# Kernel tuning notes

Measured on AMD Instinct MI355X. Metric: run time of the kernel, lower is better.

Reference implementation:

```python
import jax, jax.numpy as jnp
import numpy as np


def setup_inputs() -> dict:
    key = jax.random.key(0)
    ks = jax.random.split(key, 8)
    B, IN, P, D1, D2, C = 1024, 4096, 512, 8, 16, 4
    H1, H2 = D1 * P, D2 * P
    H3 = H2 // 4
    return {
        "data_omics": jax.random.normal(ks[0], (B, IN), jnp.float32),
        "comp": jax.random.randint(ks[1], (IN, P), 0, 2, jnp.int32),
        "fc1_w": jax.random.normal(ks[2], (IN, H1), jnp.float32) * (2.0 / (IN + H1)) ** 0.5,
        "fc1_b": jax.random.uniform(ks[3], (H1,), jnp.float32),
        "fc2_w": jax.random.normal(ks[4], (H1, H2), jnp.float32) * (2.0 / (H1 + H2)) ** 0.5,
        "fc2_b": jax.random.uniform(ks[5], (H2,), jnp.float32),
        "w3": jax.random.normal(ks[6], (H2, H3), jnp.float32) * (2.0 / (H2 + H3)) ** 0.5,
        "b3": jnp.zeros((H3,), jnp.float32),
        "w4": jax.random.normal(ks[7], (H3, C), jnp.float32) * (2.0 / (H3 + C)) ** 0.5,
        "b4": jnp.zeros((C,), jnp.float32),
    }


def reference(data_omics, comp, fc1_w, fc1_b, fc2_w, fc2_b, w3, b3, w4, b4):
    P = comp.shape[1]
    D1 = fc1_w.shape[1] // P          # dim_per_path_1
    D2 = fc2_w.shape[1] // P          # dim_per_path_2
    # mask_1: [input_dim, D1*P] gene->pathway membership, repeated per hidden unit
    mask_1 = jnp.repeat(comp.astype(fc1_w.dtype), D1, axis=1)
    # mask_2: block-diagonal [D1*P, D2*P] with D1xD2 blocks of ones
    mask_2 = jnp.kron(jnp.eye(P, dtype=fc2_w.dtype), jnp.ones((D1, D2), fc2_w.dtype))
    out = jnp.matmul(data_omics, fc1_w * mask_1) + fc1_b      # [B, D1*P]
    out = jnp.matmul(out, fc2_w * mask_2) + fc2_b             # [B, D2*P]
    h = jax.nn.relu(jnp.matmul(out, w3) + b3)                 # dropout is eval no-op
    logits = jnp.matmul(h, w4) + b4                           # [B, num_classes]
    return logits
```

## Files before the change

kernel.cpp:

```cpp
#include <hip/hip_runtime.h>
#include <hip/hip_bf16.h>
#include <cstdint>
#include <cstddef>

typedef __bf16 bf16_t;
typedef __bf16 bf16x8 __attribute__((ext_vector_type(8)));
typedef float f32x4 __attribute__((ext_vector_type(4)));

#define AS1(p) ((const __attribute__((address_space(1))) void*)(p))
#define AS3(p) ((__attribute__((address_space(3))) void*)(p))

struct bf16x4_s { bf16_t x, y, z, w; };

__global__ __launch_bounds__(256) void k_transpose(const float* __restrict__ W,
                                                   const int* __restrict__ comp,
                                                   bf16_t* __restrict__ Bt,
                                                   int K, int N, int Pc) {
  __shared__ float tile[64][65];
  const int k0 = blockIdx.x * 64;
  const int n0 = blockIdx.y * 64;
  const int t = threadIdx.x;
  const int c = t & 63;
  const int r0 = t >> 6;
#pragma unroll
  for (int i = 0; i < 16; ++i) {
    int r = r0 + i * 4;
    float v = W[(size_t)(k0 + r) * N + n0 + c];
    v *= (float)comp[(size_t)(k0 + r) * Pc + ((n0 + c) >> 3)];
    tile[r][c] = v;
  }
  __syncthreads();
#pragma unroll
  for (int i = 0; i < 16; ++i) {
    int r = r0 + i * 4;
    Bt[(size_t)(n0 + r) * K + k0 + c] = (bf16_t)tile[c][r];
  }
}

__global__ __launch_bounds__(256) void k_w23(const float* __restrict__ fc2w,
                                             const float* __restrict__ w3,
                                             const float* __restrict__ b2,
                                             bf16_t* __restrict__ W23t,
                                             float* __restrict__ b23) {
  __shared__ float w3s[128][65];
  const int n0 = blockIdx.x * 64;
  const int pb = blockIdx.y * 8;
  const int tid = threadIdx.x;
  const int c = tid & 63, q = tid >> 6;
#pragma unroll
  for (int i = 0; i < 32; ++i) {
    int rr = i * 4 + q;
    w3s[rr][c] = w3[(size_t)(pb * 16 + rr) * 2048 + n0 + c];
  }
  __syncthreads();
  const int pp = c >> 3;
  const int k1 = pb * 8 + c;
  const int p = pb + pp;
  float f2[16];
  const float4* frp = (const float4*)(fc2w + (size_t)k1 * 8192 + (size_t)p * 16);
#pragma unroll
  for (int t4 = 0; t4 < 4; ++t4) {
    float4 v = frp[t4];
    f2[t4 * 4 + 0] = v.x; f2[t4 * 4 + 1] = v.y; f2[t4 * 4 + 2] = v.z; f2[t4 * 4 + 3] = v.w;
  }
#pragma unroll
  for (int i = 0; i < 16; ++i) {
    int nn = i * 4 + q;
    float s = 0.f;
#pragma unroll
    for (int d2 = 0; d2 < 16; ++d2) {
      int d2r = (d2 + 2 * pp) & 15;
      s += f2[d2r] * w3s[pp * 16 + d2r][nn];
    }
    W23t[(size_t)(n0 + nn) * 4096 + k1] = (bf16_t)s;
  }
  float bp = 0.f;
  for (int rr = q * 32; rr < q * 32 + 32; ++rr)
    bp += b2[pb * 16 + rr] * w3s[rr][c];
  atomicAdd(&b23[n0 + c], bp);
}

template<int MI, int NI, bool AF32>
__global__ __launch_bounds__(256, 2) void k_gemm_sk(const void* __restrict__ Av,
                                                    const bf16_t* __restrict__ Bt,
                                                    float* __restrict__ P,
                                                    int M, int N, int K, int ksub) {
  constexpr int BM = MI * 32;
  constexpr int BN = NI * 32;
  constexpr int BK = 32;
  __shared__ bf16_t As[BM][BK];
  __shared__ bf16_t Bs[BN][BK];
  const int tid = threadIdx.x;
  const int wave = tid >> 6;
  const int lane = tid & 63;
  const int m0 = blockIdx.y * BM;
  const int n0 = blockIdx.x * BN;
  const int kbase = blockIdx.z * ksub;
  const int wm = (wave >> 1) * (MI * 16);
  const int wn = (wave & 1) * (NI * 16);
  const int lrow = lane >> 2;
  const int lk = (lane & 3) * 8;
  const int fr = lane & 15;
  const int fkb = (lane >> 4) * 8;

  f32x4 acc[MI][NI] = {};
  const int nkt = ksub / BK;
  for (int kt = 0; kt < nkt; ++kt) {
    const int k0 = kbase + kt * BK;
    if constexpr (AF32) {
      const float* Af = (const float*)Av;
      for (int i = wave; i < BM / 16; i += 4) {
        const float* g = Af + (size_t)(m0 + i * 16 + lrow) * K + k0 + lk;
        float4 a0 = *(const float4*)g;
        float4 a1 = *(const float4*)(g + 4);
        bf16x8 v;
        v[0] = (bf16_t)a0.x; v[1] = (bf16_t)a0.y; v[2] = (bf16_t)a0.z; v[3] = (bf16_t)a0.w;
        v[4] = (bf16_t)a1.x; v[5] = (bf16_t)a1.y; v[6] = (bf16_t)a1.z; v[7] = (bf16_t)a1.w;
        *reinterpret_cast<bf16x8*>(&As[i * 16 + lrow][lk]) = v;
      }
    } else {
      const bf16_t* Ab = (const bf16_t*)Av;
      for (int i = wave; i < BM / 16; i += 4) {
        const bf16_t* g = Ab + (size_t)(m0 + i * 16 + lrow) * K + k0 + lk;
        __builtin_amdgcn_global_load_lds(AS1(g), AS3(&As[i * 16][0]), 16, 0, 0);
      }
    }
    for (int i = wave; i < BN / 16; i += 4) {
      const bf16_t* g = Bt + (size_t)(n0 + i * 16 + lrow) * K + k0 + lk;
      __builtin_amdgcn_global_load_lds(AS1(g), AS3(&Bs[i * 16][0]), 16, 0, 0);
    }
    __syncthreads();

    bf16x8 af[MI], bfr[NI];
#pragma unroll
    for (int mi = 0; mi < MI; ++mi)
      af[mi] = *reinterpret_cast<const bf16x8*>(&As[wm + mi * 16 + fr][fkb]);
#pragma unroll
    for (int ni = 0; ni < NI; ++ni)
      bfr[ni] = *reinterpret_cast<const bf16x8*>(&Bs[wn + ni * 16 + fr][fkb]);
#pragma unroll
    for (int mi = 0; mi < MI; ++mi)
#pragma unroll
      for (int ni = 0; ni < NI; ++ni)
        acc[mi][ni] = __builtin_amdgcn_mfma_f32_16x16x32_bf16(af[mi], bfr[ni], acc[mi][ni], 0, 0, 0);
    __syncthreads();
  }

  float* Po = P + (size_t)blockIdx.z * ((size_t)M * N);
  const int fq = lane >> 4;
#pragma unroll
  for (int mi = 0; mi < MI; ++mi)
#pragma unroll
    for (int ni = 0; ni < NI; ++ni) {
      const int col = n0 + wn + ni * 16 + fr;
#pragma unroll
      for (int j = 0; j < 4; ++j) {
        const int row = m0 + wm + mi * 16 + fq * 4 + j;
        Po[(size_t)row * N + col] = acc[mi][ni][j];
      }
    }
}

template<int S, bool RELU, bool B2>
__global__ __launch_bounds__(256) void k_reduce(const float* __restrict__ P, size_t sz,
                                                const float* __restrict__ bias1,
                                                const float* __restrict__ bias2,
                                                bf16_t* __restrict__ out, int N) {
  const size_t i = (size_t)blockIdx.x * 256 + threadIdx.x;
  const size_t off = i * 4;
  float4 a = *(const float4*)(P + off);
#pragma unroll
  for (int s = 1; s < S; ++s) {
    float4 t = *(const float4*)(P + (size_t)s * sz + off);
    a.x += t.x; a.y += t.y; a.z += t.z; a.w += t.w;
  }
  const int col = (int)(off & (size_t)(N - 1));
  const float4 b1 = *(const float4*)(bias1 + col);
  a.x += b1.x; a.y += b1.y; a.z += b1.z; a.w += b1.w;
  if (B2) {
    const float4 b2v = *(const float4*)(bias2 + col);
    a.x += b2v.x; a.y += b2v.y; a.z += b2v.z; a.w += b2v.w;
  }
  if (RELU) {
    a.x = fmaxf(a.x, 0.f); a.y = fmaxf(a.y, 0.f);
    a.z = fmaxf(a.z, 0.f); a.w = fmaxf(a.w, 0.f);
  }
  bf16x4_s o{(bf16_t)a.x, (bf16_t)a.y, (bf16_t)a.z, (bf16_t)a.w};
  reinterpret_cast<bf16x4_s*>(out)[i] = o;
}

__global__ __launch_bounds__(256) void k_head(const bf16_t* __restrict__ h,
                                              const float* __restrict__ W4,
                                              const float* __restrict__ b4,
                                              float* __restrict__ out) {
  const int b = blockIdx.x;
  const int n = threadIdx.x >> 6;
  const int lane = threadIdx.x & 63;
  float s = 0.f;
  for (int k = lane; k < 2048; k += 64)
    s += (float)h[(size_t)b * 2048 + k] * W4[k * 4 + n];
#pragma unroll
  for (int off = 32; off; off >>= 1) s += __shfl_down(s, off);
  if (lane == 0) out[b * 4 + n] = s + b4[n];
}

extern "C" void kernel_launch(void* const* d_in, const int* in_sizes, int n_in,
                              void* d_out, int out_size, void* d_ws, size_t ws_size,
                              hipStream_t stream) {
  const float* data  = (const float*)d_in[0];
  const int*   comp  = (const int*)d_in[1];
  const float* fc1_w = (const float*)d_in[2];
  const float* fc1_b = (const float*)d_in[3];
  const float* fc2_w = (const float*)d_in[4];
  const float* fc2_b = (const float*)d_in[5];
  const float* w3    = (const float*)d_in[6];
  const float* b3    = (const float*)d_in[7];
  const float* w4    = (const float*)d_in[8];
  const float* b4    = (const float*)d_in[9];
  float* logits = (float*)d_out;

  char* ws = (char*)d_ws;
  bf16_t* Bt1  = (bf16_t*)(ws);
  bf16_t* out1 = (bf16_t*)(ws);
  bf16_t* W23t = (bf16_t*)(ws + 8388608);
  float*  b23  = (float*)(ws + 25165824);
  bf16_t* hbuf = (bf16_t*)(ws + 25174016);
  float*  P    = (float*)(ws + 33554432);

  k_transpose<<<dim3(64, 64), 256, 0, stream>>>(fc1_w, comp, Bt1, 4096, 4096, 512);
  k_gemm_sk<4, 4, true><<<dim3(32, 8, 2), 256, 0, stream>>>(data, Bt1, P, 1024, 4096, 4096, 2048);
  k_reduce<2, false, false><<<4096, 256, 0, stream>>>(P, (size_t)1024 * 4096, fc1_b, nullptr, out1, 4096);
  hipMemsetAsync(b23, 0, 8192, stream);
  k_w23<<<dim3(32, 64), 256, 0, stream>>>(fc2_w, w3, fc2_b, W23t, b23);
  k_gemm_sk<4, 4, false><<<dim3(16, 8, 4), 256, 0, stream>>>(out1, W23t, P, 1024, 2048, 4096, 1024);
  k_reduce<4, true, true><<<2048, 256, 0, stream>>>(P, (size_t)1024 * 2048, b23, b3, hbuf, 2048);
  k_head<<<1024, 256, 0, stream>>>(hbuf, w4, b4, logits);
}
```

Before: 458.5 us.

## Double-buffer GEMM LDS tiles, pre-cast input to bf16, deepen split-K

The split-K GEMM now double-buffers its A and B tiles in LDS, issuing the next tile's global loads before the MFMA work on the current tile. This drops one barrier per k-step and raises MFMA priority with s_setprio. When the workspace is large enough, the fp32 input is first cast to bf16 in a separate kernel so both GEMMs use the direct global-to-LDS load path. Split-K depth doubles in both GEMMs for more parallelism, at the cost of more partial-sum traffic in the reduce kernels and twice the LDS per block.

```diff
diff --git a/kernel.cpp b/kernel.cpp
--- a/kernel.cpp
+++ b/kernel.cpp
@@ -11,6 +11,16 @@
 #define AS3(p) ((__attribute__((address_space(3))) void*)(p))
 
 struct bf16x4_s { bf16_t x, y, z, w; };
+
+__global__ __launch_bounds__(256) void k_cast_bf16(const float4* __restrict__ in,
+                                                   bf16x4_s* __restrict__ out, int n4) {
+  int i = blockIdx.x * 256 + threadIdx.x;
+  if (i < n4) {
+    float4 v = in[i];
+    bf16x4_s o{(bf16_t)v.x, (bf16_t)v.y, (bf16_t)v.z, (bf16_t)v.w};
+    out[i] = o;
+  }
+}
 
 __global__ __launch_bounds__(256) void k_transpose(const float* __restrict__ W,
                                                    const int* __restrict__ comp,
@@ -81,69 +91,114 @@
 }
 
 template<int MI, int NI, bool AF32>
-__global__ __launch_bounds__(256, 2) void k_gemm_sk(const void* __restrict__ Av,
-                                                    const bf16_t* __restrict__ Bt,
-                                                    float* __restrict__ P,
-                                                    int M, int N, int K, int ksub) {
-  constexpr int BM = MI * 32;
-  constexpr int BN = NI * 32;
-  constexpr int BK = 32;
-  __shared__ bf16_t As[BM][BK];
-  __shared__ bf16_t Bs[BN][BK];
-  const int tid = threadIdx.x;
-  const int wave = tid >> 6;
-  const int lane = tid & 63;
-  const int m0 = blockIdx.y * BM;
-  const int n0 = blockIdx.x * BN;
+__global__ __launch_bounds__(256, AF32 ? 2 : 4)
+void k_gemm_sk(const void* __restrict__ Av,
+               const bf16_t* __restrict__ Bt,
+               float* __restrict__ P,
+               int M, int N, int K, int ksub) {
+  constexpr int BM = MI * 32, BN = NI * 32, BK = 32;
+  constexpr int AIT = BM / 64;
+  constexpr int BIT = BN / 64;
+  __shared__ bf16_t As[2][BM][BK];
+  __shared__ bf16_t Bs[2][BN][BK];
+  const int tid = threadIdx.x, wave = tid >> 6, lane = tid & 63;
+  const int m0 = blockIdx.y * BM, n0 = blockIdx.x * BN;
   const int kbase = blockIdx.z * ksub;
-  const int wm = (wave >> 1) * (MI * 16);
-  const int wn = (wave & 1) * (NI * 16);
-  const int lrow = lane >> 2;
-  const int lk = (lane & 3) * 8;
-  const int fr = lane & 15;
-  const int fkb = (lane >> 4) * 8;
+  const int wm = (wave >> 1) * (MI * 16), wn = (wave & 1) * (NI * 16);
+  const int lrow = lane >> 2, lk = (lane & 3) * 8;
+  const int fr = lane & 15, fkb = (lane >> 4) * 8;
+  const float* Af = (const float*)Av;
+  const bf16_t* Ab = (const bf16_t*)Av;
 
   f32x4 acc[MI][NI] = {};
   const int nkt = ksub / BK;
+
+  if constexpr (AF32) {
+#pragma unroll
+    for (int ii = 0; ii < AIT; ++ii) {
+      const int i = wave + ii * 4;
+      const float* g = Af + (size_t)(m0 + i * 16 + lrow) * K + kbase + lk;
+      float4 x = *(const float4*)g, y = *(const float4*)(g + 4);
+      bf16x8 v;
+      v[0] = (bf16_t)x.x; v[1] = (bf16_t)x.y; v[2] = (bf16_t)x.z; v[3] = (bf16_t)x.w;
+      v[4] = (bf16_t)y.x; v[5] = (bf16_t)y.y; v[6] = (bf16_t)y.z; v[7] = (bf16_t)y.w;
+      *reinterpret_cast<bf16x8*>(&As[0][i * 16 + lrow][lk]) = v;
+    }
+  } else {
+#pragma unroll
+    for (int ii = 0; ii < AIT; ++ii) {
+      const int i = wave + ii * 4;
+      const bf16_t* g = Ab + (size_t)(m0 + i * 16 + lrow) * K + kbase + lk;
+      __builtin_amdgcn_global_load_lds(AS1(g), AS3(&As[0][i * 16][0]), 16, 0, 0);
+    }
+  }
+#pragma unroll
+  for (int ii = 0; ii < BIT; ++ii) {
+    const int i = wave + ii * 4;
+    const bf16_t* g = Bt + (size_t)(n0 + i * 16 + lrow) * K + kbase + lk;
+    __builtin_amdgcn_global_load_lds(AS1(g), AS3(&Bs[0][i * 16][0]), 16, 0, 0);
+  }
+  __syncthreads();
+
+  int cur = 0;
   for (int kt = 0; kt < nkt; ++kt) {
-    const int k0 = kbase + kt * BK;
-    if constexpr (AF32) {
-      const float* Af = (const float*)Av;
-      for (int i = wave; i < BM / 16; i += 4) {
-        const float* g = Af + (size_t)(m0 + i * 16 + lrow) * K + k0 + lk;
-        float4 a0 = *(const float4*)g;
-        float4 a1 = *(const float4*)(g + 4);
-        bf16x8 v;
-        v[0] = (bf16_t)a0.x; v[1] = (bf16_t)a0.y; v[2] = (bf16_t)a0.z; v[3] = (bf16_t)a0.w;
-        v[4] = (bf16_t)a1.x; v[5] = (bf16_t)a1.y; v[6] = (bf16_t)a1.z; v[7] = (bf16_t)a1.w;
-        *reinterpret_cast<bf16x8*>(&As[i * 16 + lrow][lk]) = v;
+    const bool pf = (kt + 1 < nkt);
+    const int k1 = kbase + (kt + 1) * BK;
+    float4 ax[AIT], ay[AIT];
+    if (pf) {
+      if constexpr (AF32) {
+#pragma unroll
+        for (int ii = 0; ii < AIT; ++ii) {
+          const int i = wave + ii * 4;
+          const float* g = Af + (size_t)(m0 + i * 16 + lrow) * K + k1 + lk;
+          ax[ii] = *(const float4*)g;
+          ay[ii] = *(const float4*)(g + 4);
+        }
+      } else {
+#pragma unroll
+        for (int ii = 0; ii < AIT; ++ii) {
+          const int i = wave + ii * 4;
+          const bf16_t* g = Ab + (size_t)(m0 + i * 16 + lrow) * K + k1 + lk;
+          __builtin_amdgcn_global_load_lds(AS1(g), AS3(&As[cur ^ 1][i * 16][0]), 16, 0, 0);
+        }
       }
-    } else {
-      const bf16_t* Ab = (const bf16_t*)Av;
-      for (int i = wave; i < BM / 16; i += 4) {
-        const bf16_t* g = Ab + (size_t)(m0 + i * 16 + lrow) * K + k0 + lk;
-        __builtin_amdgcn_global_load_lds(AS1(g), AS3(&As[i * 16][0]), 16, 0, 0);
+#pragma unroll
+      for (int ii = 0; ii < BIT; ++ii) {
+        const int i = wave + ii * 4;
+        const bf16_t* g = Bt + (size_t)(n0 + i * 16 + lrow) * K + k1 + lk;
+        __builtin_amdgcn_global_load_lds(AS1(g), AS3(&Bs[cur ^ 1][i * 16][0]), 16, 0, 0);
       }
     }
-    for (int i = wave; i < BN / 16; i += 4) {
-      const bf16_t* g = Bt + (size_t)(n0 + i * 16 + lrow) * K + k0 + lk;
-      __builtin_amdgcn_global_load_lds(AS1(g), AS3(&Bs[i * 16][0]), 16, 0, 0);
-    }
-    __syncthreads();
 
     bf16x8 af[MI], bfr[NI];
 #pragma unroll
     for (int mi = 0; mi < MI; ++mi)
-      af[mi] = *reinterpret_cast<const bf16x8*>(&As[wm + mi * 16 + fr][fkb]);
+      af[mi] = *reinterpret_cast<const bf16x8*>(&As[cur][wm + mi * 16 + fr][fkb]);
 #pragma unroll
     for (int ni = 0; ni < NI; ++ni)
-      bfr[ni] = *reinterpret_cast<const bf16x8*>(&Bs[wn + ni * 16 + fr][fkb]);
+      bfr[ni] = *reinterpret_cast<const bf16x8*>(&Bs[cur][wn + ni * 16 + fr][fkb]);
+    __builtin_amdgcn_s_setprio(1);
 #pragma unroll
     for (int mi = 0; mi < MI; ++mi)
 #pragma unroll
       for (int ni = 0; ni < NI; ++ni)
         acc[mi][ni] = __builtin_amdgcn_mfma_f32_16x16x32_bf16(af[mi], bfr[ni], acc[mi][ni], 0, 0, 0);
+    __builtin_amdgcn_s_setprio(0);
+
+    if (pf) {
+      if constexpr (AF32) {
+#pragma unroll
+        for (int ii = 0; ii < AIT; ++ii) {
+          const int i = wave + ii * 4;
+          bf16x8 v;
+          v[0] = (bf16_t)ax[ii].x; v[1] = (bf16_t)ax[ii].y; v[2] = (bf16_t)ax[ii].z; v[3] = (bf16_t)ax[ii].w;
+          v[4] = (bf16_t)ay[ii].x; v[5] = (bf16_t)ay[ii].y; v[6] = (bf16_t)ay[ii].z; v[7] = (bf16_t)ay[ii].w;
+          *reinterpret_cast<bf16x8*>(&As[cur ^ 1][i * 16 + lrow][lk]) = v;
+        }
+      }
+    }
     __syncthreads();
+    cur ^= 1;
   }
 
   float* Po = P + (size_t)blockIdx.z * ((size_t)M * N);
@@ -220,19 +275,42 @@
   float* logits = (float*)d_out;
 
   char* ws = (char*)d_ws;
-  bf16_t* Bt1  = (bf16_t*)(ws);
-  bf16_t* out1 = (bf16_t*)(ws);
-  bf16_t* W23t = (bf16_t*)(ws + 8388608);
-  float*  b23  = (float*)(ws + 25165824);
-  bf16_t* hbuf = (bf16_t*)(ws + 25174016);
-  float*  P    = (float*)(ws + 33554432);
-
-  k_transpose<<<dim3(64, 64), 256, 0, stream>>>(fc1_w, comp, Bt1, 4096, 4096, 512);
-  k_gemm_sk<4, 4, true><<<dim3(32, 8, 2), 256, 0, stream>>>(data, Bt1, P, 1024, 4096, 4096, 2048);
-  k_reduce<2, false, false><<<4096, 256, 0, stream>>>(P, (size_t)1024 * 4096, fc1_b, nullptr, out1, 4096);
-  hipMemsetAsync(b23, 0, 8192, stream);
-  k_w23<<<dim3(32, 64), 256, 0, stream>>>(fc2_w, w3, fc2_b, W23t, b23);
-  k_gemm_sk<4, 4, false><<<dim3(16, 8, 4), 256, 0, stream>>>(out1, W23t, P, 1024, 2048, 4096, 1024);
-  k_reduce<4, true, true><<<2048, 256, 0, stream>>>(P, (size_t)1024 * 2048, b23, b3, hbuf, 2048);
-  k_head<<<1024, 256, 0, stream>>>(hbuf, w4, b4, logits);
-}
+  const size_t MB = 1024 * 1024;
+  const bool big = ws_size >= 104 * MB;
+
+  if (big) {
+    bf16_t* dataB = (bf16_t*)(ws);
+    bf16_t* Bt1   = (bf16_t*)(ws + 8 * MB);
+    float*  P     = (float*)(ws + 40 * MB);
+    bf16_t* out1  = (bf16_t*)(ws);
+    bf16_t* W23t  = (bf16_t*)(ws + 8 * MB);
+    float*  b23   = (float*)(ws + 24 * MB);
+    bf16_t* hbuf  = (bf16_t*)(ws + 24 * MB + 65536);
+
+    k_cast_bf16<<<4096, 256, 0, stream>>>((const float4*)data, (bf16x4_s*)dataB, 1048576);
+    k_transpose<<<dim3(64, 64), 256, 0, stream>>>(fc1_w, comp, Bt1, 4096, 4096, 512);
+    k_gemm_sk<4, 4, false><<<dim3(32, 8, 4), 256, 0, stream>>>(dataB, Bt1, P, 1024, 4096, 4096, 1024);
+    k_reduce<4, false, false><<<4096, 256, 0, stream>>>(P, (size_t)1024 * 4096, fc1_b, nullptr, out1, 4096);
+    hipMemsetAsync(b23, 0, 8192, stream);
+    k_w23<<<dim3(32, 64), 256, 0, stream>>>(fc2_w, w3, fc2_b, W23t, b23);
+    k_gemm_sk<4, 4, false><<<dim3(16, 8, 8), 256, 0, stream>>>(out1, W23t, P, 1024, 2048, 4096, 512);
+    k_reduce<8, true, true><<<2048, 256, 0, stream>>>(P, (size_t)1024 * 2048, b23, b3, hbuf, 2048);
+    k_head<<<1024, 256, 0, stream>>>(hbuf, w4, b4, logits);
+  } else {
+    bf16_t* Bt1   = (bf16_t*)(ws);
+    float*  P     = (float*)(ws + 32 * MB);
+    bf16_t* out1  = (bf16_t*)(ws);
+    bf16_t* W23t  = (bf16_t*)(ws + 8 * MB);
+    float*  b23   = (float*)(ws + 24 * MB);
+    bf16_t* hbuf  = (bf16_t*)(ws + 24 * MB + 65536);
+
+    k_transpose<<<dim3(64, 64), 256, 0, stream>>>(fc1_w, comp, Bt1, 4096, 4096, 512);
+    k_gemm_sk<4, 4, true><<<dim3(32, 8, 2), 256, 0, stream>>>(data, Bt1, P, 1024, 4096, 4096, 2048);
+    k_reduce<2, false, false><<<4096, 256, 0, stream>>>(P, (size_t)1024 * 4096, fc1_b, nullptr, out1, 4096);
+    hipMemsetAsync(b23, 0, 8192, stream);
+    k_w23<<<dim3(32, 64), 256, 0, stream>>>(fc2_w, w3, fc2_b, W23t, b23);
+    k_gemm_sk<4, 4, false><<<dim3(16, 8, 4), 256, 0, stream>>>(out1, W23t, P, 1024, 2048, 4096, 1024);
+    k_reduce<4, true, true><<<2048, 256, 0, stream>>>(P, (size_t)1024 * 2048, b23, b3, hbuf, 2048);
+    k_head<<<1024, 256, 0, stream>>>(hbuf, w4, b4, logits);
+  }
+}
```

Measured after the change: 400.7 us. 1.14x faster.
